# Kernel tuning notes

Hardware: AMD Instinct MI355X
Metric: run time of the kernel (lower is better)

The kernel has to match this reference:

```python
import jax, jax.numpy as jnp
import numpy as np

FEAT_DIM = 256
NUM_HEADS = 8
HEAD_DIM = FEAT_DIM // NUM_HEADS
N_NODES = 4096
LN_EPS = 1e-5


def setup_inputs() -> dict:
    key = jax.random.key(0)
    ks = jax.random.split(key, 10)
    C = FEAT_DIM
    s = 1.0 / np.sqrt(C)
    x = jax.random.normal(ks[0], (N_NODES, C), dtype=jnp.float32)
    Wq = jax.random.uniform(ks[1], (C, C), jnp.float32, -s, s)
    bq = jax.random.uniform(ks[2], (C,), jnp.float32, -s, s)
    Wk = jax.random.uniform(ks[3], (C, C), jnp.float32, -s, s)
    bk = jax.random.uniform(ks[4], (C,), jnp.float32, -s, s)
    Wv = jax.random.uniform(ks[5], (C, C), jnp.float32, -s, s)
    bv = jax.random.uniform(ks[6], (C,), jnp.float32, -s, s)
    Wo = jax.random.uniform(ks[7], (C, C), jnp.float32, -s, s)
    bo = jax.random.uniform(ks[8], (C,), jnp.float32, -s, s)
    scale = jnp.float32(1.0 / np.sqrt(HEAD_DIM))
    gamma = jnp.ones((C,), jnp.float32)
    beta = jnp.zeros((C,), jnp.float32)
    return {"x": x, "Wq": Wq, "bq": bq, "Wk": Wk, "bk": bk, "Wv": Wv,
            "bv": bv, "scale": scale, "Wo": Wo, "bo": bo,
            "gamma": gamma, "beta": beta}


def reference(x, Wq, bq, Wk, bk, Wv, bv, scale, Wo, bo, gamma, beta):
    N, C = x.shape
    H, D = NUM_HEADS, HEAD_DIM
    q = (x @ Wq + bq).reshape(N, H, D)
    k = (x @ Wk + bk).reshape(N, H, D)
    v = (x @ Wv + bv).reshape(N, H, D)
    # scores[i, j, h]; softmax over j (the key/node axis), per original dim=1
    scores = jnp.einsum('ihd,jhd->ijh', q, k) * scale
    attn = jax.nn.softmax(scores, axis=1)
    messages = jnp.einsum('ijh,jhd->ihd', attn, v).reshape(N, H * D)
    y = x + messages @ Wo + bo
    # LayerNorm over last dim
    mu = jnp.mean(y, axis=-1, keepdims=True)
    var = jnp.mean(jnp.square(y - mu), axis=-1, keepdims=True)
    return (y - mu) * jax.lax.rsqrt(var + LN_EPS) * gamma + beta
```

## Files before the change

### kernel.cpp

```cpp
#include <hip/hip_runtime.h>
#include <hip/hip_bf16.h>
#include <math.h>

#define NN 4096
#define C  256
#define NH 8
#define HD 32
#define LN_EPS 1e-5f
#define LOG2E 1.44269504088896340736f

typedef unsigned short u16;
typedef __attribute__((ext_vector_type(8))) short bf16x8;
typedef __attribute__((ext_vector_type(4))) float f32x4;
typedef __attribute__((ext_vector_type(16))) float f32x16;

__device__ inline u16 f2b(float f) {
    union { float f; unsigned u; } v; v.f = f;
    unsigned r = (v.u + 0x7fff + ((v.u >> 16) & 1)) >> 16;
    return (u16)r;
}

__device__ inline float fexp2(float x) {
#if __has_builtin(__builtin_amdgcn_exp2f)
    return __builtin_amdgcn_exp2f(x);
#else
    return exp2f(x);
#endif
}

__device__ inline unsigned pack_trunc(float e0, float e1) {
    return __builtin_amdgcn_perm(__float_as_uint(e1), __float_as_uint(e0),
                                 0x07060302u);
}

__device__ inline void atomic_add_agent(float* p, float v) {
    __hip_atomic_fetch_add(p, v, __ATOMIC_RELAXED, __HIP_MEMORY_SCOPE_AGENT);
}

__device__ inline f32x16 zero16() {
    return f32x16{0.f,0.f,0.f,0.f, 0.f,0.f,0.f,0.f,
                  0.f,0.f,0.f,0.f, 0.f,0.f,0.f,0.f};
}

template<int c>
__device__ inline bf16x8 softmax_chunk(const f32x16 s, float& lsum) {
    const float e0 = fexp2(s[8*c+0]);
    const float e1 = fexp2(s[8*c+1]);
    const float e2 = fexp2(s[8*c+2]);
    const float e3 = fexp2(s[8*c+3]);
    const float e4 = fexp2(s[8*c+4]);
    const float e5 = fexp2(s[8*c+5]);
    const float e6 = fexp2(s[8*c+6]);
    const float e7 = fexp2(s[8*c+7]);
    lsum += ((e0 + e1) + (e2 + e3)) + ((e4 + e5) + (e6 + e7));
    const unsigned p01 = pack_trunc(e0, e1);
    const unsigned p23 = pack_trunc(e2, e3);
    const unsigned p45 = pack_trunc(e4, e5);
    const unsigned p67 = pack_trunc(e6, e7);
    const auto w02 = __builtin_amdgcn_permlane32_swap(p01, p45, false, false);
    const auto w13 = __builtin_amdgcn_permlane32_swap(p23, p67, false, false);
    union { unsigned w[4]; bf16x8 v; } pa;
    pa.w[0] = w02[0]; pa.w[1] = w13[0];
    pa.w[2] = w02[1]; pa.w[3] = w13[1];
    return pa.v;
}

__global__ __launch_bounds__(256) void prep_kernel(
    const float* __restrict__ Wq, const float* __restrict__ Wk,
    const float* __restrict__ Wv, const float* __restrict__ Wo,
    const float* __restrict__ x,
    u16* __restrict__ WqkvT, u16* __restrict__ WoT, u16* __restrict__ xb)
{
    const int z = blockIdx.z;
    if (z < 4) {
        __shared__ float tile[32][33];
        const float* W = (z == 0) ? Wq : (z == 1) ? Wk : (z == 2) ? Wv : Wo;
        u16* WT = (z == 3) ? WoT : (WqkvT + (size_t)z * 256 * 256);
        const int tx = threadIdx.x & 31, ty = threadIdx.x >> 5;
        const int n0 = blockIdx.x * 32, k0 = blockIdx.y * 32;
        #pragma unroll
        for (int i = 0; i < 32; i += 8)
            tile[ty + i][tx] = W[(size_t)(k0 + ty + i) * 256 + n0 + tx];
        __syncthreads();
        #pragma unroll
        for (int i = 0; i < 32; i += 8)
            WT[(size_t)(n0 + ty + i) * 256 + k0 + tx] = f2b(tile[tx][ty + i]);
    } else {
        const int slice = z - 4;
        const int bid = blockIdx.x * 8 + blockIdx.y;
        const int base = slice * (NN * C / 4) + bid * 4096 + threadIdx.x * 16;
        #pragma unroll
        for (int i = 0; i < 4; ++i) {
            const float4 v = *(const float4*)(x + base + i * 4);
            union { u16 u[4]; unsigned long long ull; } pk;
            pk.u[0] = f2b(v.x); pk.u[1] = f2b(v.y);
            pk.u[2] = f2b(v.z); pk.u[3] = f2b(v.w);
            *(unsigned long long*)(xb + base + i * 4) = pk.ull;
        }
    }
}

__global__ __launch_bounds__(256) void qkv_mfma_kernel(
    const u16* __restrict__ xb, const u16* __restrict__ WT,
    const float* __restrict__ bq, const float* __restrict__ bk,
    const float* __restrict__ bv, const float* __restrict__ scale_p,
    u16* __restrict__ qb, u16* __restrict__ kb, u16* __restrict__ vT)
{
    const int m0 = blockIdx.x * 64;
    const int n0 = blockIdx.y * 64;
    const int t = threadIdx.x;
    const int wave = t >> 6, lane = t & 63;
    const int l16 = lane & 15, quad = lane >> 4;

    f32x4 acc[4];
    #pragma unroll
    for (int ct = 0; ct < 4; ++ct) acc[ct] = f32x4{0.f, 0.f, 0.f, 0.f};

    const u16* xrow = xb + (size_t)(m0 + wave * 16 + l16) * C;
    #pragma unroll
    for (int kk = 0; kk < 8; ++kk) {
        const bf16x8 af = *(const bf16x8*)(xrow + kk * 32 + quad * 8);
        #pragma unroll
        for (int ct = 0; ct < 4; ++ct) {
            const bf16x8 bfr = *(const bf16x8*)(
                WT + (size_t)(n0 + ct * 16 + l16) * C + kk * 32 + quad * 8);
            acc[ct] = __builtin_amdgcn_mfma_f32_16x16x32_bf16(af, bfr, acc[ct], 0, 0, 0);
        }
    }

    const int sect = n0 >> 8;
    const int c0 = n0 & 255;
    const int rbase = m0 + wave * 16 + quad * 4;
    if (sect == 0) {
        const float scl = (*scale_p) * LOG2E;
        #pragma unroll
        for (int ct = 0; ct < 4; ++ct) {
            const int c = c0 + ct * 16 + l16;
            const float b = bq[c];
            #pragma unroll
            for (int r = 0; r < 4; ++r)
                qb[(size_t)(rbase + r) * C + c] = f2b((acc[ct][r] + b) * scl);
        }
    } else if (sect == 1) {
        #pragma unroll
        for (int ct = 0; ct < 4; ++ct) {
            const int c = c0 + ct * 16 + l16;
            const float b = bk[c];
            #pragma unroll
            for (int r = 0; r < 4; ++r)
                kb[(size_t)(rbase + r) * C + c] = f2b(acc[ct][r] + b);
        }
    } else {
        #pragma unroll
        for (int ct = 0; ct < 4; ++ct) {
            const int c = c0 + ct * 16 + l16;
            const float b = bv[c];
            union { u16 u[4]; unsigned long long ull; } pk;
            #pragma unroll
            for (int r = 0; r < 4; ++r) pk.u[r] = f2b(acc[ct][r] + b);
            *(unsigned long long*)(vT + (size_t)c * NN + rbase) = pk.ull;
        }
    }
}

#define NZ 8
#define ZT (NN / NZ)
#define TQB 256
#define NIT (ZT / 64)

__global__ __launch_bounds__(256) void attn_mfma_kernel(
    const u16* __restrict__ q, const u16* __restrict__ k,
    const u16* __restrict__ vT, float* __restrict__ msgacc,
    float* __restrict__ lacc)
{
    __shared__ u16 Ks[2][2048];
    __shared__ u16 Vs[2][2048];

    const int h = blockIdx.y, z = blockIdx.z;
    const int t = threadIdx.x;
    const int w = t >> 6, lane = t & 63;
    const int l31 = lane & 31, hi = lane >> 5;
    const int qbase = blockIdx.x * TQB + w * 64;

    const u16* qrpA = q + (size_t)(qbase + l31) * C + h * HD + hi * 8;
    const bf16x8 qf0a = *(const bf16x8*)(qrpA);
    const bf16x8 qf1a = *(const bf16x8*)(qrpA + 16);
    const u16* qrpB = qrpA + 32 * C;
    const bf16x8 qf0b = *(const bf16x8*)(qrpB);
    const bf16x8 qf1b = *(const bf16x8*)(qrpB + 16);

    f32x16 oA = zero16(), oB = zero16();
    float lsA = 0.f, lsB = 0.f;

    const int sst = w >> 1, sfc = w & 1;
    const u16* gk = k + (size_t)(z * ZT + sst * 32 + l31) * C
                      + h * HD + sfc * 16 + hi * 8;
    const u16* gv = vT + (size_t)(h * HD + l31) * NN
                       + z * ZT + sst * 32 + sfc * 16 + hi * 8;

    bf16x8 kreg = *(const bf16x8*)(gk);
    bf16x8 vreg = *(const bf16x8*)(gv);

    for (int it = 0; it < NIT; ++it) {
        const int b = it & 1;
        *(bf16x8*)(&Ks[b][w * 512 + lane * 8]) = kreg;
        *(bf16x8*)(&Vs[b][w * 512 + lane * 8]) = vreg;
        __syncthreads();

        if (it + 1 < NIT) {
            kreg = *(const bf16x8*)(gk + (size_t)(it + 1) * 64 * C);
            vreg = *(const bf16x8*)(gv + (it + 1) * 64);
        }

        const u16* KsB = Ks[b];
        const u16* VsB = Vs[b];
        #pragma unroll
        for (int s = 0; s < 2; ++s) {
            const bf16x8 kf0 = *(const bf16x8*)(KsB + (s * 2 + 0) * 512 + lane * 8);
            const bf16x8 kf1 = *(const bf16x8*)(KsB + (s * 2 + 1) * 512 + lane * 8);
            const bf16x8 vf0 = *(const bf16x8*)(VsB + (s * 2 + 0) * 512 + lane * 8);
            const bf16x8 vf1 = *(const bf16x8*)(VsB + (s * 2 + 1) * 512 + lane * 8);

            f32x16 sA = zero16();
            sA = __builtin_amdgcn_mfma_f32_32x32x16_bf16(kf0, qf0a, sA, 0, 0, 0);
            sA = __builtin_amdgcn_mfma_f32_32x32x16_bf16(kf1, qf1a, sA, 0, 0, 0);
            const bf16x8 paA0 = softmax_chunk<0>(sA, lsA);
            oA = __builtin_amdgcn_mfma_f32_32x32x16_bf16(paA0, vf0, oA, 0, 0, 0);
            const bf16x8 paA1 = softmax_chunk<1>(sA, lsA);
            oA = __builtin_amdgcn_mfma_f32_32x32x16_bf16(paA1, vf1, oA, 0, 0, 0);

            f32x16 sB = zero16();
            sB = __builtin_amdgcn_mfma_f32_32x32x16_bf16(kf0, qf0b, sB, 0, 0, 0);
            sB = __builtin_amdgcn_mfma_f32_32x32x16_bf16(kf1, qf1b, sB, 0, 0, 0);
            const bf16x8 paB0 = softmax_chunk<0>(sB, lsB);
            oB = __builtin_amdgcn_mfma_f32_32x32x16_bf16(paB0, vf0, oB, 0, 0, 0);
            const bf16x8 paB1 = softmax_chunk<1>(sB, lsB);
            oB = __builtin_amdgcn_mfma_f32_32x32x16_bf16(paB1, vf1, oB, 0, 0, 0);
        }
        __syncthreads();
    }

    lsA += __shfl_xor(lsA, 32);
    lsB += __shfl_xor(lsB, 32);
    if (hi == 0) {
        atomic_add_agent(&lacc[(size_t)(qbase + l31) * NH + h], lsA);
        atomic_add_agent(&lacc[(size_t)(qbase + 32 + l31) * NH + h], lsB);
    }

    #pragma unroll
    for (int r = 0; r < 16; ++r) {
        const int qrA = qbase + (r & 3) + 8 * (r >> 2) + 4 * hi;
        atomic_add_agent(&msgacc[(size_t)qrA * C + h * HD + l31], oA[r]);
        atomic_add_agent(&msgacc[(size_t)(qrA + 32) * C + h * HD + l31], oB[r]);
    }
}

#define OROWS 8
__global__ __launch_bounds__(256) void out_ln_mfma_kernel(
    const float* __restrict__ msgacc, const float* __restrict__ lacc,
    const u16* __restrict__ WoT, const float* __restrict__ bo,
    const float* __restrict__ x, const float* __restrict__ gamma,
    const float* __restrict__ beta, float* __restrict__ out)
{
    __shared__ float sums[2][4][OROWS];
    const int m0 = blockIdx.x * OROWS;
    const int t = threadIdx.x;
    const int w = t >> 6, lane = t & 63;
    const int l16 = lane & 15, quad = lane >> 4;

    f32x4 acc[4];
    #pragma unroll
    for (int ct = 0; ct < 4; ++ct) acc[ct] = f32x4{0.f, 0.f, 0.f, 0.f};

    const int ar = min(m0 + l16, NN - 1);
    const float* arow = msgacc + (size_t)ar * C;
    const float* lrow = lacc + (size_t)ar * NH;
    #pragma unroll
    for (int kk = 0; kk < 8; ++kk) {
        const float li = 1.f / lrow[kk];
        const float4 a0 = *(const float4*)(arow + kk * 32 + quad * 8);
        const float4 a1 = *(const float4*)(arow + kk * 32 + quad * 8 + 4);
        union { __hip_bfloat162 h2[4]; bf16x8 v; } af;
        af.h2[0] = __float22bfloat162_rn(float2{a0.x * li, a0.y * li});
        af.h2[1] = __float22bfloat162_rn(float2{a0.z * li, a0.w * li});
        af.h2[2] = __float22bfloat162_rn(float2{a1.x * li, a1.y * li});
        af.h2[3] = __float22bfloat162_rn(float2{a1.z * li, a1.w * li});
        #pragma unroll
        for (int ct = 0; ct < 4; ++ct) {
            const bf16x8 bfr = *(const bf16x8*)(
                WoT + (size_t)(w * 64 + ct * 16 + l16) * C + kk * 32 + quad * 8);
            acc[ct] = __builtin_amdgcn_mfma_f32_16x16x32_bf16(af.v, bfr, acc[ct], 0, 0, 0);
        }
    }

    float val[4][4];
    if (quad < 2) {
        #pragma unroll
        for (int r = 0; r < 4; ++r) {
            const int row = m0 + quad * 4 + r;
            float sr = 0.f, qr = 0.f;
            #pragma unroll
            for (int ct = 0; ct < 4; ++ct) {
                const int c = w * 64 + ct * 16 + l16;
                const float v = acc[ct][r] + bo[c] + x[(size_t)row * C + c];
                val[ct][r] = v;
                sr += v;
                qr = fmaf(v, v, qr);
            }
            sr += __shfl_xor(sr, 1); sr += __shfl_xor(sr, 2);
            sr += __shfl_xor(sr, 4); sr += __shfl_xor(sr, 8);
            qr += __shfl_xor(qr, 1); qr += __shfl_xor(qr, 2);
            qr += __shfl_xor(qr, 4); qr += __shfl_xor(qr, 8);
            if (l16 == 0) {
                sums[0][w][quad * 4 + r] = sr;
                sums[1][w][quad * 4 + r] = qr;
            }
        }
    }
    __syncthreads();

    if (quad < 2) {
        #pragma unroll
        for (int r = 0; r < 4; ++r) {
            const int ri = quad * 4 + r;
            const int row = m0 + ri;
            const float tot  = sums[0][0][ri] + sums[0][1][ri] + sums[0][2][ri] + sums[0][3][ri];
            const float tot2 = sums[1][0][ri] + sums[1][1][ri] + sums[1][2][ri] + sums[1][3][ri];
            const float mu = tot * (1.f / C);
            const float var = fmaxf(tot2 * (1.f / C) - mu * mu, 0.f);
            const float rstd = rsqrtf(var + LN_EPS);
            #pragma unroll
            for (int ct = 0; ct < 4; ++ct) {
                const int c = w * 64 + ct * 16 + l16;
                out[(size_t)row * C + c] = (val[ct][r] - mu) * rstd * gamma[c] + beta[c];
            }
        }
    }
}

extern "C" void kernel_launch(void* const* d_in, const int* in_sizes, int n_in,
                              void* d_out, int out_size, void* d_ws, size_t ws_size,
                              hipStream_t stream) {
    const float* x     = (const float*)d_in[0];
    const float* Wq    = (const float*)d_in[1];
    const float* bq    = (const float*)d_in[2];
    const float* Wk    = (const float*)d_in[3];
    const float* bk    = (const float*)d_in[4];
    const float* Wv    = (const float*)d_in[5];
    const float* bv    = (const float*)d_in[6];
    const float* scale = (const float*)d_in[7];
    const float* Wo    = (const float*)d_in[8];
    const float* bo    = (const float*)d_in[9];
    const float* gamma = (const float*)d_in[10];
    const float* beta  = (const float*)d_in[11];
    float* out = (float*)d_out;

    u16* qb     = (u16*)d_ws;
    u16* kb     = qb + (size_t)NN * C;
    u16* vT     = kb + (size_t)NN * C;
    u16* xbuf   = vT + (size_t)NN * C;
    u16* WqkvT  = xbuf + (size_t)NN * C;
    u16* WoT    = WqkvT + (size_t)3 * C * C;
    float* msgacc = (float*)(WoT + (size_t)C * C);
    float* lacc   = msgacc + (size_t)NN * C;

    hipMemsetAsync(msgacc, 0, ((size_t)NN * C + (size_t)NN * NH) * sizeof(float),
                   stream);

    prep_kernel<<<dim3(8, 8, 8), 256, 0, stream>>>(Wq, Wk, Wv, Wo, x,
                                                   WqkvT, WoT, xbuf);
    qkv_mfma_kernel<<<dim3(NN / 64, 12), 256, 0, stream>>>(
        xbuf, WqkvT, bq, bk, bv, scale, qb, kb, vT);
    attn_mfma_kernel<<<dim3(NN / TQB, NH, NZ), 256, 0, stream>>>(
        qb, kb, vT, msgacc, lacc);
    out_ln_mfma_kernel<<<NN / OROWS, 256, 0, stream>>>(msgacc, lacc, WoT, bo, x,
                                                       gamma, beta, out);
}
```

Baseline: 161.1 us.

## Replace atomic split-K attention reduction with partial buffers and fuse x conversion

The attention kernel now writes per-split partial message and row-sum buffers, using 4 key splits instead of 8 and 128 queries per block, rather than atomically accumulating into a zeroed buffer. The output kernel sums these partials itself. This removes the memset and the heavy global atomic traffic. The x-to-bf16 conversion moves from the prep kernel into the QKV GEMM's A-operand load, dropping a pass over x. In exchange the output kernel reads four partial buffers, there are more attention blocks each doing half the query work, and the QKV kernel reads fp32 x.

```diff
diff --git a/kernel.cpp b/kernel.cpp
--- a/kernel.cpp
+++ b/kernel.cpp
@@ -9,6 +9,11 @@
 #define LN_EPS 1e-5f
 #define LOG2E 1.44269504088896340736f
 
+#define NZ 4
+#define ZT (NN / NZ)
+#define TQB 128
+#define NIT (ZT / 64)
+
 typedef unsigned short u16;
 typedef __attribute__((ext_vector_type(8))) short bf16x8;
 typedef __attribute__((ext_vector_type(4))) float f32x4;
@@ -31,10 +36,6 @@
 __device__ inline unsigned pack_trunc(float e0, float e1) {
     return __builtin_amdgcn_perm(__float_as_uint(e1), __float_as_uint(e0),
                                  0x07060302u);
-}
-
-__device__ inline void atomic_add_agent(float* p, float v) {
-    __hip_atomic_fetch_add(p, v, __ATOMIC_RELAXED, __HIP_MEMORY_SCOPE_AGENT);
 }
 
 __device__ inline f32x16 zero16() {
@@ -68,40 +69,25 @@
 __global__ __launch_bounds__(256) void prep_kernel(
     const float* __restrict__ Wq, const float* __restrict__ Wk,
     const float* __restrict__ Wv, const float* __restrict__ Wo,
-    const float* __restrict__ x,
-    u16* __restrict__ WqkvT, u16* __restrict__ WoT, u16* __restrict__ xb)
+    u16* __restrict__ WqkvT, u16* __restrict__ WoT)
 {
+    __shared__ float tile[32][33];
     const int z = blockIdx.z;
-    if (z < 4) {
-        __shared__ float tile[32][33];
-        const float* W = (z == 0) ? Wq : (z == 1) ? Wk : (z == 2) ? Wv : Wo;
-        u16* WT = (z == 3) ? WoT : (WqkvT + (size_t)z * 256 * 256);
-        const int tx = threadIdx.x & 31, ty = threadIdx.x >> 5;
-        const int n0 = blockIdx.x * 32, k0 = blockIdx.y * 32;
-        #pragma unroll
-        for (int i = 0; i < 32; i += 8)
-            tile[ty + i][tx] = W[(size_t)(k0 + ty + i) * 256 + n0 + tx];
-        __syncthreads();
-        #pragma unroll
-        for (int i = 0; i < 32; i += 8)
-            WT[(size_t)(n0 + ty + i) * 256 + k0 + tx] = f2b(tile[tx][ty + i]);
-    } else {
-        const int slice = z - 4;
-        const int bid = blockIdx.x * 8 + blockIdx.y;
-        const int base = slice * (NN * C / 4) + bid * 4096 + threadIdx.x * 16;
-        #pragma unroll
-        for (int i = 0; i < 4; ++i) {
-            const float4 v = *(const float4*)(x + base + i * 4);
-            union { u16 u[4]; unsigned long long ull; } pk;
-            pk.u[0] = f2b(v.x); pk.u[1] = f2b(v.y);
-            pk.u[2] = f2b(v.z); pk.u[3] = f2b(v.w);
-            *(unsigned long long*)(xb + base + i * 4) = pk.ull;
-        }
-    }
+    const float* W = (z == 0) ? Wq : (z == 1) ? Wk : (z == 2) ? Wv : Wo;
+    u16* WT = (z == 3) ? WoT : (WqkvT + (size_t)z * 256 * 256);
+    const int tx = threadIdx.x & 31, ty = threadIdx.x >> 5;
+    const int n0 = blockIdx.x * 32, k0 = blockIdx.y * 32;
+    #pragma unroll
+    for (int i = 0; i < 32; i += 8)
+        tile[ty + i][tx] = W[(size_t)(k0 + ty + i) * 256 + n0 + tx];
+    __syncthreads();
+    #pragma unroll
+    for (int i = 0; i < 32; i += 8)
+        WT[(size_t)(n0 + ty + i) * 256 + k0 + tx] = f2b(tile[tx][ty + i]);
 }
 
 __global__ __launch_bounds__(256) void qkv_mfma_kernel(
-    const u16* __restrict__ xb, const u16* __restrict__ WT,
+    const float* __restrict__ x, const u16* __restrict__ WT,
     const float* __restrict__ bq, const float* __restrict__ bk,
     const float* __restrict__ bv, const float* __restrict__ scale_p,
     u16* __restrict__ qb, u16* __restrict__ kb, u16* __restrict__ vT)
@@ -116,15 +102,21 @@
     #pragma unroll
     for (int ct = 0; ct < 4; ++ct) acc[ct] = f32x4{0.f, 0.f, 0.f, 0.f};
 
-    const u16* xrow = xb + (size_t)(m0 + wave * 16 + l16) * C;
+    const float* xrow = x + (size_t)(m0 + wave * 16 + l16) * C;
     #pragma unroll
     for (int kk = 0; kk < 8; ++kk) {
-        const bf16x8 af = *(const bf16x8*)(xrow + kk * 32 + quad * 8);
+        const float4 a0 = *(const float4*)(xrow + kk * 32 + quad * 8);
+        const float4 a1 = *(const float4*)(xrow + kk * 32 + quad * 8 + 4);
+        union { __hip_bfloat162 h2[4]; bf16x8 v; } af;
+        af.h2[0] = __float22bfloat162_rn(float2{a0.x, a0.y});
+        af.h2[1] = __float22bfloat162_rn(float2{a0.z, a0.w});
+        af.h2[2] = __float22bfloat162_rn(float2{a1.x, a1.y});
+        af.h2[3] = __float22bfloat162_rn(float2{a1.z, a1.w});
         #pragma unroll
         for (int ct = 0; ct < 4; ++ct) {
             const bf16x8 bfr = *(const bf16x8*)(
                 WT + (size_t)(n0 + ct * 16 + l16) * C + kk * 32 + quad * 8);
-            acc[ct] = __builtin_amdgcn_mfma_f32_16x16x32_bf16(af, bfr, acc[ct], 0, 0, 0);
+            acc[ct] = __builtin_amdgcn_mfma_f32_16x16x32_bf16(af.v, bfr, acc[ct], 0, 0, 0);
         }
     }
 
@@ -163,15 +155,10 @@
     }
 }
 
-#define NZ 8
-#define ZT (NN / NZ)
-#define TQB 256
-#define NIT (ZT / 64)
-
 __global__ __launch_bounds__(256) void attn_mfma_kernel(
     const u16* __restrict__ q, const u16* __restrict__ k,
-    const u16* __restrict__ vT, float* __restrict__ msgacc,
-    float* __restrict__ lacc)
+    const u16* __restrict__ vT, float* __restrict__ msgp,
+    float* __restrict__ lp)
 {
     __shared__ u16 Ks[2][2048];
     __shared__ u16 Vs[2][2048];
@@ -180,17 +167,14 @@
     const int t = threadIdx.x;
     const int w = t >> 6, lane = t & 63;
     const int l31 = lane & 31, hi = lane >> 5;
-    const int qbase = blockIdx.x * TQB + w * 64;
-
-    const u16* qrpA = q + (size_t)(qbase + l31) * C + h * HD + hi * 8;
-    const bf16x8 qf0a = *(const bf16x8*)(qrpA);
-    const bf16x8 qf1a = *(const bf16x8*)(qrpA + 16);
-    const u16* qrpB = qrpA + 32 * C;
-    const bf16x8 qf0b = *(const bf16x8*)(qrpB);
-    const bf16x8 qf1b = *(const bf16x8*)(qrpB + 16);
-
-    f32x16 oA = zero16(), oB = zero16();
-    float lsA = 0.f, lsB = 0.f;
+    const int qbase = blockIdx.x * TQB + w * 32;
+
+    const u16* qrp = q + (size_t)(qbase + l31) * C + h * HD + hi * 8;
+    const bf16x8 qf0 = *(const bf16x8*)(qrp);
+    const bf16x8 qf1 = *(const bf16x8*)(qrp + 16);
+
+    f32x16 o = zero16();
+    float lsum = 0.f;
 
     const int sst = w >> 1, sfc = w & 1;
     const u16* gk = k + (size_t)(z * ZT + sst * 32 + l31) * C
@@ -222,42 +206,30 @@
             const bf16x8 vf1 = *(const bf16x8*)(VsB + (s * 2 + 1) * 512 + lane * 8);
 
             f32x16 sA = zero16();
-            sA = __builtin_amdgcn_mfma_f32_32x32x16_bf16(kf0, qf0a, sA, 0, 0, 0);
-            sA = __builtin_amdgcn_mfma_f32_32x32x16_bf16(kf1, qf1a, sA, 0, 0, 0);
-            const bf16x8 paA0 = softmax_chunk<0>(sA, lsA);
-            oA = __builtin_amdgcn_mfma_f32_32x32x16_bf16(paA0, vf0, oA, 0, 0, 0);
-            const bf16x8 paA1 = softmax_chunk<1>(sA, lsA);
-            oA = __builtin_amdgcn_mfma_f32_32x32x16_bf16(paA1, vf1, oA, 0, 0, 0);
-
-            f32x16 sB = zero16();
-            sB = __builtin_amdgcn_mfma_f32_32x32x16_bf16(kf0, qf0b, sB, 0, 0, 0);
-            sB = __builtin_amdgcn_mfma_f32_32x32x16_bf16(kf1, qf1b, sB, 0, 0, 0);
-            const bf16x8 paB0 = softmax_chunk<0>(sB, lsB);
-            oB = __builtin_amdgcn_mfma_f32_32x32x16_bf16(paB0, vf0, oB, 0, 0, 0);
-            const bf16x8 paB1 = softmax_chunk<1>(sB, lsB);
-            oB = __builtin_amdgcn_mfma_f32_32x32x16_bf16(paB1, vf1, oB, 0, 0, 0);
+            sA = __builtin_amdgcn_mfma_f32_32x32x16_bf16(kf0, qf0, sA, 0, 0, 0);
+            sA = __builtin_amdgcn_mfma_f32_32x32x16_bf16(kf1, qf1, sA, 0, 0, 0);
+            const bf16x8 pa0 = softmax_chunk<0>(sA, lsum);
+            o = __builtin_amdgcn_mfma_f32_32x32x16_bf16(pa0, vf0, o, 0, 0, 0);
+            const bf16x8 pa1 = softmax_chunk<1>(sA, lsum);
+            o = __builtin_amdgcn_mfma_f32_32x32x16_bf16(pa1, vf1, o, 0, 0, 0);
         }
         __syncthreads();
     }
 
-    lsA += __shfl_xor(lsA, 32);
-    lsB += __shfl_xor(lsB, 32);
-    if (hi == 0) {
-        atomic_add_agent(&lacc[(size_t)(qbase + l31) * NH + h], lsA);
-        atomic_add_agent(&lacc[(size_t)(qbase + 32 + l31) * NH + h], lsB);
-    }
+    lsum += __shfl_xor(lsum, 32);
+    if (hi == 0)
+        lp[((size_t)z * NH + h) * NN + qbase + l31] = lsum;
 
     #pragma unroll
     for (int r = 0; r < 16; ++r) {
-        const int qrA = qbase + (r & 3) + 8 * (r >> 2) + 4 * hi;
-        atomic_add_agent(&msgacc[(size_t)qrA * C + h * HD + l31], oA[r]);
-        atomic_add_agent(&msgacc[(size_t)(qrA + 32) * C + h * HD + l31], oB[r]);
+        const int qr = qbase + (r & 3) + 8 * (r >> 2) + 4 * hi;
+        msgp[((size_t)z * NN + qr) * C + h * HD + l31] = o[r];
     }
 }
 
 #define OROWS 8
 __global__ __launch_bounds__(256) void out_ln_mfma_kernel(
-    const float* __restrict__ msgacc, const float* __restrict__ lacc,
+    const float* __restrict__ msgp, const float* __restrict__ lp,
     const u16* __restrict__ WoT, const float* __restrict__ bo,
     const float* __restrict__ x, const float* __restrict__ gamma,
     const float* __restrict__ beta, float* __restrict__ out)
@@ -273,13 +245,25 @@
     for (int ct = 0; ct < 4; ++ct) acc[ct] = f32x4{0.f, 0.f, 0.f, 0.f};
 
     const int ar = min(m0 + l16, NN - 1);
-    const float* arow = msgacc + (size_t)ar * C;
-    const float* lrow = lacc + (size_t)ar * NH;
     #pragma unroll
     for (int kk = 0; kk < 8; ++kk) {
-        const float li = 1.f / lrow[kk];
-        const float4 a0 = *(const float4*)(arow + kk * 32 + quad * 8);
-        const float4 a1 = *(const float4*)(arow + kk * 32 + quad * 8 + 4);
+        float l = 0.f;
+        #pragma unroll
+        for (int z = 0; z < NZ; ++z)
+            l += lp[((size_t)z * NH + kk) * NN + ar];
+        const float li = 1.f / l;
+
+        float4 a0 = float4{0.f, 0.f, 0.f, 0.f};
+        float4 a1 = float4{0.f, 0.f, 0.f, 0.f};
+        #pragma unroll
+        for (int z = 0; z < NZ; ++z) {
+            const float* arow = msgp + ((size_t)z * NN + ar) * C;
+            const float4 b0 = *(const float4*)(arow + kk * 32 + quad * 8);
+            const float4 b1 = *(const float4*)(arow + kk * 32 + quad * 8 + 4);
+            a0.x += b0.x; a0.y += b0.y; a0.z += b0.z; a0.w += b0.w;
+            a1.x += b1.x; a1.y += b1.y; a1.z += b1.z; a1.w += b1.w;
+        }
+
         union { __hip_bfloat162 h2[4]; bf16x8 v; } af;
         af.h2[0] = __float22bfloat162_rn(float2{a0.x * li, a0.y * li});
         af.h2[1] = __float22bfloat162_rn(float2{a0.z * li, a0.w * li});
@@ -358,21 +342,17 @@
     u16* qb     = (u16*)d_ws;
     u16* kb     = qb + (size_t)NN * C;
     u16* vT     = kb + (size_t)NN * C;
-    u16* xbuf   = vT + (size_t)NN * C;
-    u16* WqkvT  = xbuf + (size_t)NN * C;
+    u16* WqkvT  = vT + (size_t)NN * C;
     u16* WoT    = WqkvT + (size_t)3 * C * C;
-    float* msgacc = (float*)(WoT + (size_t)C * C);
-    float* lacc   = msgacc + (size_t)NN * C;
-
-    hipMemsetAsync(msgacc, 0, ((size_t)NN * C + (size_t)NN * NH) * sizeof(float),
-                   stream);
-
-    prep_kernel<<<dim3(8, 8, 8), 256, 0, stream>>>(Wq, Wk, Wv, Wo, x,
-                                                   WqkvT, WoT, xbuf);
+    float* msgp = (float*)(WoT + (size_t)C * C);
+    float* lp   = msgp + (size_t)NZ * NN * C;
+
+    prep_kernel<<<dim3(8, 8, 4), 256, 0, stream>>>(Wq, Wk, Wv, Wo,
+                                                   WqkvT, WoT);
     qkv_mfma_kernel<<<dim3(NN / 64, 12), 256, 0, stream>>>(
-        xbuf, WqkvT, bq, bk, bv, scale, qb, kb, vT);
+        x, WqkvT, bq, bk, bv, scale, qb, kb, vT);
     attn_mfma_kernel<<<dim3(NN / TQB, NH, NZ), 256, 0, stream>>>(
-        qb, kb, vT, msgacc, lacc);
-    out_ln_mfma_kernel<<<NN / OROWS, 256, 0, stream>>>(msgacc, lacc, WoT, bo, x,
+        qb, kb, vT, msgp, lp);
+    out_ln_mfma_kernel<<<NN / OROWS, 256, 0, stream>>>(msgp, lp, WoT, bo, x,
                                                        gamma, beta, out);
 }
```

Result: faster. 154.0 us (-4.5%).
